# Kernel optimization log

Measured on AMD Instinct MI355X. Metric: run time of the kernel, lower is better.

Reference implementation:

```python
import jax, jax.numpy as jnp
import numpy as np

V, E, H = 32000, 256, 512   # vocab, embed_dim, hidden_dim
B, S, T = 16, 512, 128      # batch, src_len, tgt_len
PAD = 0
H2 = 2 * H                  # decoder hidden size


def setup_inputs() -> dict:
    key = jax.random.key(0)
    ks = jax.random.split(key, 20)
    g = lambda k, shape: jax.random.normal(k, shape, dtype=jnp.float32) * 0.05
    emb = g(ks[0], (V, E)).at[PAD].set(0.0)  # padding_idx row zeroed
    inp = {
        "src": jax.random.randint(ks[18], (B, S), 0, V, dtype=jnp.int32),
        "tgt": jax.random.randint(ks[19], (B, T), 0, V, dtype=jnp.int32),
        "emb": emb,
        # encoder forward direction (torch gate order i,f,g,o)
        "Wih_f": g(ks[1], (4 * H, E)), "Whh_f": g(ks[2], (4 * H, H)),
        "bih_f": g(ks[3], (4 * H,)),   "bhh_f": g(ks[4], (4 * H,)),
        # encoder backward direction
        "Wih_b": g(ks[5], (4 * H, E)), "Whh_b": g(ks[6], (4 * H, H)),
        "bih_b": g(ks[7], (4 * H,)),   "bhh_b": g(ks[8], (4 * H,)),
        # decoder LSTM: input E+2H, hidden 2H
        "Wih_d": g(ks[9], (4 * H2, E + H2)), "Whh_d": g(ks[10], (4 * H2, H2)),
        "bih_d": g(ks[11], (4 * H2,)),       "bhh_d": g(ks[12], (4 * H2,)),
        # attention Linear(4H -> 2H)
        "Wa": g(ks[13], (H2, 2 * H2)), "ba": g(ks[14], (H2,)),
        # output Linear(2H -> V)
        "Wo": g(ks[15], (V, H2)), "bo": g(ks[16], (V,)),
    }
    return inp


def _lstm_cell(x, h, c, Wih, Whh, bih, bhh):
    z = x @ Wih.T + h @ Whh.T + bih + bhh
    i, f, g, o = jnp.split(z, 4, axis=-1)
    c = jax.nn.sigmoid(f) * c + jax.nn.sigmoid(i) * jnp.tanh(g)
    h = jax.nn.sigmoid(o) * jnp.tanh(c)
    return h, c


def _lstm_scan(xs, h0, c0, Wih, Whh, bih, bhh):
    def step(carry, x):
        h, c = _lstm_cell(x, carry[0], carry[1], Wih, Whh, bih, bhh)
        return (h, c), h
    (hT, cT), hs = jax.lax.scan(step, (h0, c0), xs)
    return hs, hT, cT


def reference(src, tgt, emb, Wih_f, Whh_f, bih_f, bhh_f, Wih_b, Whh_b, bih_b, bhh_b,
              Wih_d, Whh_d, bih_d, bhh_d, Wa, ba, Wo, bo):
    z = jnp.zeros((B, H), dtype=emb.dtype)
    xs = emb[src].transpose(1, 0, 2)                       # [S,B,E]
    hs_f, hTf, _ = _lstm_scan(xs,        z, z, Wih_f, Whh_f, bih_f, bhh_f)
    hs_b, hTb, _ = _lstm_scan(xs[::-1],  z, z, Wih_b, Whh_b, bih_b, bhh_b)
    enc_out = jnp.concatenate([hs_f, hs_b[::-1]], -1).transpose(1, 0, 2)  # [B,S,2H]
    h = jnp.concatenate([hTf, hTb], -1)                    # decoder h0 [B,2H]
    c = jnp.zeros_like(h)  # note: original reuses encoder c_n; see combined c0 below
    # original uses c_n (last cells) as decoder c0:
    _, _, cTf = _lstm_scan(xs, z, z, Wih_f, Whh_f, bih_f, bhh_f)[1], None, None
    # recompute cleanly (scan already returned cT above; redo properly):
    hs_f2, hTf2, cTf2 = _lstm_scan(xs,       z, z, Wih_f, Whh_f, bih_f, bhh_f)
    hs_b2, hTb2, cTb2 = _lstm_scan(xs[::-1], z, z, Wih_b, Whh_b, bih_b, bhh_b)
    c = jnp.concatenate([cTf2, cTb2], -1)

    Wa_h, Wa_e = Wa[:, :H2], Wa[:, H2:]
    enc_proj = jnp.einsum('bsd,kd->bsk', enc_out, Wa_e) + ba  # [B,S,2H]

    dec_xs = emb[tgt[:, :T - 1]].transpose(1, 0, 2)        # [T-1,B,E] teacher-forced

    def dec_step(carry, x):
        h, c = carry
        energy = jnp.tanh(enc_proj + (h @ Wa_h.T)[:, None, :])  # [B,S,2H]
        w = jax.nn.softmax(energy.sum(-1), axis=1)              # [B,S]
        ctx = jnp.einsum('bs,bsd->bd', w, enc_out)              # [B,2H]
        xi = jnp.concatenate([x, ctx], -1)                      # [B,E+2H]
        h, c = _lstm_cell(xi, h, c, Wih_d, Whh_d, bih_d, bhh_d)
        pred = h @ Wo.T + bo                                    # [B,V]
        return (h, c), pred

    _, preds = jax.lax.scan(dec_step, (h, c), dec_xs)           # [T-1,B,V]
    outputs = jnp.concatenate(
        [jnp.zeros((B, 1, V), dtype=preds.dtype), preds.transpose(1, 0, 2)], axis=1)
    return outputs
```

## Files before the change

### kernel.cpp

```cpp
#include <hip/hip_runtime.h>

typedef unsigned int uint;
typedef unsigned short ushort;
typedef unsigned long long ull;
typedef __attribute__((ext_vector_type(8))) short bf16x8;
typedef __attribute__((ext_vector_type(4))) float f32x4;

static constexpr int V_ = 32000, E_ = 256, H_ = 512, B_ = 16, S_ = 512, T_ = 128;
static constexpr int H2_ = 1024, G4_ = 2048, D4_ = 4096, KXI_ = 2304;
static constexpr int DSTEPS = T_ - 1;
static constexpr int MD = 2048;
static constexpr int NWG_DEC = 256;
static constexpr float LOG2E = 1.4426950408889634f;
static constexpr int ASTR = 2312;

#define DEVFN __device__ __forceinline__

DEVFN ushort f2bf(float f){ uint u = __builtin_bit_cast(uint, f); u += 0x7fffu + ((u>>16)&1u); return (ushort)(u>>16); }
DEVFN float bf2f(ushort h){ uint u = ((uint)h)<<16; return __builtin_bit_cast(float, u); }
DEVFN float fsig(float x){ float e = __builtin_amdgcn_exp2f(-LOG2E*x); return __builtin_amdgcn_rcpf(1.f+e); }
DEVFN float ftanh(float x){ x = fminf(15.f,fmaxf(-15.f,x)); float e = __builtin_amdgcn_exp2f(2.f*LOG2E*x); return (e-1.f)*__builtin_amdgcn_rcpf(e+1.f); }
DEVFN f32x4 mfma16(bf16x8 a, bf16x8 b, f32x4 c){ return __builtin_amdgcn_mfma_f32_16x16x32_bf16(a,b,c,0,0,0); }

struct ull2v{ ull x, y; };
DEVFN ull ald64(const void* p){ return __hip_atomic_load((const ull*)p, __ATOMIC_RELAXED, __HIP_MEMORY_SCOPE_AGENT); }
DEVFN uint ald32u(const uint* p){ return __hip_atomic_load(p, __ATOMIC_RELAXED, __HIP_MEMORY_SCOPE_AGENT); }
DEVFN float ald_f32(const float* p){ uint v = __hip_atomic_load((const uint*)p, __ATOMIC_RELAXED, __HIP_MEMORY_SCOPE_AGENT); return __builtin_bit_cast(float, v); }
DEVFN bf16x8 ald_bf16x8(const ushort* p){ ull2v v{ald64(p), ald64(p+4)}; return __builtin_bit_cast(bf16x8, v); }
DEVFN void ast32(float* p, float v){ __hip_atomic_store(p, v, __ATOMIC_RELAXED, __HIP_MEMORY_SCOPE_AGENT); }
DEVFN void ast16(ushort* p, ushort v){ __hip_atomic_store(p, v, __ATOMIC_RELAXED, __HIP_MEMORY_SCOPE_AGENT); }
DEVFN void astu(uint* p, uint v){ __hip_atomic_store(p, v, __ATOMIC_RELAXED, __HIP_MEMORY_SCOPE_AGENT); }

DEVFN void gbar(uint* flags, int wgid, int tid, uint& rnd){
  __syncthreads();
  rnd++;
  if (tid==0) astu(flags + wgid, rnd);
  if (tid<256){
    while (ald32u(flags + tid) < rnd) __builtin_amdgcn_s_sleep(1);
  }
  __syncthreads();
}
DEVFN void lbar(uint* lflags, int grp, int mem, int tid, uint& rnd){
  __syncthreads();
  rnd++;
  if (tid==0) astu(lflags + grp*16 + mem, rnd);
  if (tid<16){
    while (ald32u(lflags + grp*16 + tid) < rnd) __builtin_amdgcn_s_sleep(1);
  }
  __syncthreads();
}

__global__ void k_init(uint* __restrict__ flags, ushort* __restrict__ hgf, ushort* __restrict__ hgb){
  int i = blockIdx.x*256 + threadIdx.x;
  if (i < 1024) flags[i] = 0;
  if (i < 2*B_*H_){ hgf[i]=0; hgb[i]=0; }
}

__global__ void k_embed(const int* __restrict__ src, const int* __restrict__ tgt,
                        const float* __restrict__ emb, ushort* __restrict__ Xb, ushort* __restrict__ DXb){
  int r = blockIdx.x, tid = threadIdx.x;
  if (r < S_*B_){
    int s = r>>4, b = r&15;
    int id = src[b*S_+s];
    Xb[(size_t)r*E_+tid] = f2bf(emb[(size_t)id*E_+tid]);
  } else {
    int r2 = r - S_*B_;
    int t = r2>>4, b = r2&15;
    int id = tgt[b*T_+t];
    DXb[(size_t)r2*E_+tid] = f2bf(emb[(size_t)id*E_+tid]);
  }
}

__global__ void k_cvt_encw(const float* __restrict__ src, ushort* __restrict__ dst){
  int d = blockIdx.x;
  int wg = d>>7, r = d&127;
  int w = r>>4, jj=(r>>2)&3, g=r&3;
  int srow = g*H_ + wg*32 + w*4 + jj;
  for (int c = threadIdx.x; c < E_; c += 256)
    dst[(size_t)d*E_ + c] = f2bf(src[(size_t)srow*E_ + c]);
}

__global__ void k_bias_encp(const float* __restrict__ bih, const float* __restrict__ bhh, float* __restrict__ dst){
  int d = blockIdx.x*256 + threadIdx.x;
  int wg = d>>7, r = d&127;
  int w = r>>4, jj=(r>>2)&3, g=r&3;
  int srow = g*H_ + wg*32 + w*4 + jj;
  dst[d] = bih[srow]+bhh[srow];
}

__global__ void k_cvt_decw(const float* __restrict__ Wih_d, const float* __restrict__ Whh_d,
                           ushort* __restrict__ dst){
  int d = blockIdx.x;
  int wg = d>>4, r = d&15, jj = r>>2, g = r&3;
  int srow = g*H2_ + wg*4 + jj;
  for (int c = threadIdx.x; c < KXI_; c += 256){
    float v = (c < E_+H2_) ? Wih_d[(size_t)srow*(E_+H2_) + c] : Whh_d[(size_t)srow*H2_ + (c - (E_+H2_))];
    dst[(size_t)d*KXI_ + c] = f2bf(v);
  }
}

__global__ void k_bias_decp(const float* __restrict__ bih, const float* __restrict__ bhh, float* __restrict__ dst){
  int d = blockIdx.x*256 + threadIdx.x;
  int wg = d>>4, r = d&15, jj = r>>2, g = r&3;
  int srow = g*H2_ + wg*4 + jj;
  dst[d] = bih[srow]+bhh[srow];
}

__global__ void k_cvt_strided(const float* __restrict__ src, ushort* __restrict__ dst,
                              int cols, int sld, int soff, int dld, int doff){
  int r = blockIdx.x;
  for (int c = threadIdx.x; c < cols; c += 256)
    dst[(size_t)r*dld + doff + c] = f2bf(src[(size_t)r*sld + soff + c]);
}

__global__ void k_zero_t0(float* __restrict__ out){
  int i = blockIdx.x*256 + threadIdx.x;
  if (i < B_*V_){ int b = i / V_, v = i - b*V_; out[(size_t)b*T_*V_ + v] = 0.f; }
}

template<int MODE>
__global__ __launch_bounds__(256) void gemm128(const ushort* __restrict__ A, const ushort* __restrict__ Bm,
    const float* __restrict__ bias, void* __restrict__ outp, int M, int N, int K, int Mvalid){
  __shared__ __align__(16) ushort As[128*32];
  __shared__ __align__(16) ushort Bs[128*32];
  int tid = threadIdx.x;
  int wave = tid>>6, lane = tid&63;
  int m0 = blockIdx.y*128, n0 = blockIdx.x*128;
  int wm = wave>>1, wn = wave&1;
  int col = lane&15, rg = lane>>4;
  f32x4 acc[4][4];
  #pragma unroll
  for (int i=0;i<4;i++)
    #pragma unroll
    for (int j=0;j<4;j++) acc[i][j] = {0.f,0.f,0.f,0.f};
  for (int k0=0;k0<K;k0+=32){
    __syncthreads();
    #pragma unroll
    for (int j=0;j<2;j++){
      int li = j*256+tid;
      int row = li>>2, ko = (li&3)*8;
      *(bf16x8*)(As + li*8) = *(const bf16x8*)(A + (size_t)(m0+row)*K + k0 + ko);
      *(bf16x8*)(Bs + li*8) = *(const bf16x8*)(Bm + (size_t)(n0+row)*K + k0 + ko);
    }
    __syncthreads();
    bf16x8 af[4], bfr[4];
    #pragma unroll
    for (int f=0;f<4;f++){
      af[f]  = *(const bf16x8*)(As + (wm*64+f*16+col)*32 + rg*8);
      bfr[f] = *(const bf16x8*)(Bs + (wn*64+f*16+col)*32 + rg*8);
    }
    #pragma unroll
    for (int fm=0;fm<4;fm++)
      #pragma unroll
      for (int fn=0;fn<4;fn++)
        acc[fm][fn] = mfma16(af[fm], bfr[fn], acc[fm][fn]);
  }
  #pragma unroll
  for (int fm=0;fm<4;fm++){
    int mrow = m0 + wm*64 + fm*16 + rg*4;
    #pragma unroll
    for (int fn=0;fn<4;fn++){
      int gcol = n0 + wn*64 + fn*16 + col;
      float bv = bias ? bias[gcol] : 0.f;
      #pragma unroll
      for (int i=0;i<4;i++){
        float v = acc[fm][fn][i] + bv;
        int grow = mrow + i;
        if (MODE==0) ((float*)outp)[(size_t)grow*N + gcol] = v;
        else if (MODE==1) ((ushort*)outp)[(size_t)grow*N + gcol] = f2bf(v);
        else if (MODE==3) ((ushort*)outp)[(size_t)(grow>>4)*(16*2048) + gcol*16 + (grow&15)] = f2bf(v);
        else { if (grow < Mvalid){ int b = grow&15, t = grow>>4;
               ((float*)outp)[(size_t)b*T_*V_ + (size_t)(t+1)*V_ + gcol] = v; } }
      }
    }
  }
}

__global__ __launch_bounds__(512) void k_enc_persist(
    const ushort* __restrict__ Xgf, const ushort* __restrict__ Xgb,
    const float* __restrict__ Whhf, const float* __restrict__ Whhb,
    ushort* __restrict__ enc, ushort* __restrict__ enct,
    ushort* __restrict__ hbuf1, float* __restrict__ cbuf0,
    ushort* __restrict__ hgf, ushort* __restrict__ hgb,
    uint* __restrict__ flags){
  const int dir = blockIdx.x >> 4;
  const int wg  = blockIdx.x & 15;
  const ushort* Xg = dir ? Xgb : Xgf;
  const float* Whh = dir ? Whhb : Whhf;
  ushort* hg = dir ? hgb : hgf;
  uint* ef = flags + 512 + dir*16;
  __shared__ __align__(16) ushort Wlds[128*512];
  __shared__ __align__(16) ushort hls[16*512];
  int tid = threadIdx.x;
  for (int it=0; it<32; ++it){
    int r = it*4 + (tid>>7), ct = tid&127;
    int w_ = r>>4, jj=(r>>2)&3, g=r&3;
    int srow = g*H_ + wg*32 + w_*4 + jj;
    float4 v = *(const float4*)(Whh + (size_t)srow*H_ + ct*4);
    ushort4 o; o.x=f2bf(v.x); o.y=f2bf(v.y); o.z=f2bf(v.z); o.w=f2bf(v.w);
    int byte = (r*1024 + ct*8) ^ ((r&7)<<4);
    *(ushort4*)((char*)Wlds + byte) = o;
  }
  int w = tid>>6, lane = tid&63, colL = lane&15, rg = lane>>4;
  int gg = colL&3;
  uint rnd = 0;
  float cst[4];
  #pragma unroll
  for (int i=0;i<4;i++) cst[i]=0.f;
  __syncthreads();
  for (int t=0;t<S_;++t){
    int pos = dir ? (S_-1-t) : t;
    const ushort* hsrc = hg + (t&1)*B_*H_;
    bf16x8 hv[2];
    #pragma unroll
    for (int k2=0;k2<2;k2++){
      int idx = tid + k2*512;
      hv[k2] = ald_bf16x8(hsrc + (idx>>6)*H_ + (idx&63)*8);
    }
    int colg = wg*128 + w*16 + colL;
    ushort4 xv = *(const ushort4*)(Xg + ((size_t)pos*2048 + colg)*16 + rg*4);
    f32x4 acc;
    acc[0]=bf2f(xv.x); acc[1]=bf2f(xv.y); acc[2]=bf2f(xv.z); acc[3]=bf2f(xv.w);
    #pragma unroll
    for (int k2=0;k2<2;k2++){
      int idx = tid + k2*512;
      int byte = ((idx>>6)*1024 + (idx&63)*16) ^ (((idx>>6)&7)<<4);
      *(bf16x8*)((char*)hls + byte) = hv[k2];
    }
    __syncthreads();
    int rowb = w*16 + colL;
    int base = rowb*1024 + rg*16, xm = (rowb&7)<<4;
    int hbase = colL*1024 + rg*16, hxm = (colL&7)<<4;
    #pragma unroll
    for (int kt=0;kt<16;kt++){
      bf16x8 afv = *(const bf16x8*)((const char*)hls + ((hbase + kt*64) ^ hxm));
      bf16x8 bfv = *(const bf16x8*)((const char*)Wlds + ((base + kt*64) ^ xm));
      acc = mfma16(afv, bfv, acc);
    }
    ushort* hdst = hg + ((t+1)&1)*B_*H_;
    #pragma unroll
    for (int i=0;i<4;i++){
      float v0 = acc[i];
      float v1 = __shfl_xor(v0, 1);
      float v2 = __shfl_xor(v0, 2);
      float v3 = __shfl_xor(v1, 2);
      float zi = gg==0?v0: gg==1?v1: gg==2?v2: v3;
      float zf = (gg^1)==0?v0: (gg^1)==1?v1: (gg^1)==2?v2: v3;
      float zg = (gg^2)==0?v0: (gg^2)==1?v1: (gg^2)==2?v2: v3;
      float zo = (gg^3)==0?v0: (gg^3)==1?v1: (gg^3)==2?v2: v3;
      float cc = fsig(zf)*cst[i] + fsig(zi)*ftanh(zg);
      cst[i] = cc;
      float h = fsig(zo)*ftanh(cc);
      if (gg==0){
        int j = wg*32 + w*4 + (colL>>2);
        int b = rg*4+i;
        ushort hb = f2bf(h);
        enc[((size_t)b*S_ + pos)*H2_ + dir*H_ + j] = hb;
        enct[((size_t)b*H2_ + dir*H_ + j)*S_ + pos] = hb;
        ast16(&hdst[b*H_ + j], hb);
        if (t==S_-1){
          hbuf1[b*H2_ + dir*H_ + j] = hb;
          cbuf0[b*H2_ + dir*H_ + j] = cc;
        }
      }
    }
    if (t != S_-1){
      __syncthreads();
      rnd++;
      if (tid==0) astu(ef + wg, rnd);
      if (tid<16){
        while (ald32u(ef + tid) < rnd) __builtin_amdgcn_s_sleep(1);
      }
      __syncthreads();
    }
  }
}

__global__ __launch_bounds__(512) void k_dec(
    const float* __restrict__ P, const ushort* __restrict__ WaH,
    const ushort* __restrict__ Wd, const float* __restrict__ bsd,
    const ushort* __restrict__ enct, const ushort* __restrict__ DXb,
    const float* __restrict__ cbuf0, ushort* __restrict__ hbuf,
    ushort* __restrict__ ctxbuf, float* __restrict__ qbuf,
    float* __restrict__ scores, ushort* __restrict__ hsd,
    uint* __restrict__ flags){
  __shared__ __align__(16) ushort AB[16*ASTR];
  __shared__ __align__(16) float pr[8*256];
  __shared__ float redz[256];
  __shared__ float qls[1024];
  __shared__ float wls[512];
  __shared__ float part[512];
  __shared__ float red[16];
  __shared__ float cst[64];
  uint* lflags = flags + 256;
  int wgid = blockIdx.x, tid = threadIdx.x;
  int w = tid>>6, lane = tid&63, colL = lane&15, rg = lane>>4;
  uint rnd = 0;
  if (tid < 64){
    int jj = tid>>4, b = tid&15;
    cst[tid] = cbuf0[b*H2_ + wgid*4 + jj];
  }
  for (int st=0; st<DSTEPS; ++st){
    ushort* hprev = hbuf + ((st+1)&1)*B_*H2_;
    if (wgid >= 64 && wgid < 128){
      int n0 = (wgid-64)*16;
      bf16x8 af[4];
      #pragma unroll
      for (int kt=0;kt<4;kt++)
        af[kt] = ald_bf16x8(hprev + colL*H2_ + w*128 + kt*32 + rg*8);
      f32x4 acc = {0.f,0.f,0.f,0.f};
      const ushort* Bp = WaH + (size_t)(n0+colL)*H2_ + w*128 + rg*8;
      #pragma unroll
      for (int kt=0;kt<4;kt++)
        acc = mfma16(af[kt], *(const bf16x8*)(Bp + kt*32), acc);
      *(f32x4*)&pr[w*256 + lane*4] = acc;
      __syncthreads();
      if (tid < 256){
        float s = pr[tid];
        #pragma unroll
        for (int w8=1;w8<8;w8++) s += pr[w8*256 + tid];
        int l = tid>>2, i = tid&3;
        ast32(&qbuf[(size_t)((l>>4)*4 + i)*H2_ + n0 + (l&15)], s);
      }
    }
    gbar(flags, wgid, tid, rnd);
    {
      int b = wgid>>4, wc = wgid&15;
      ull q2 = ald64((const ull*)(qbuf + (size_t)b*H2_) + tid);
      *(ull*)&qls[tid*2] = q2;
      __syncthreads();
      f32x4 qv[4];
      #pragma unroll
      for (int u=0;u<4;u++) qv[u] = *(const f32x4*)&qls[lane*16 + u*4];
      int rbase = b*S_ + wc*32 + w*4;
      #pragma unroll
      for (int rr=0;rr<4;rr++){
        int r = rbase + rr;
        const float4* Pr = (const float4*)(P + (size_t)r*H2_) + lane*4;
        float s = 0.f;
        #pragma unroll
        for (int u=0;u<4;u++){
          float4 pv = Pr[u];
          s += ftanh(pv.x+qv[u][0])+ftanh(pv.y+qv[u][1])+ftanh(pv.z+qv[u][2])+ftanh(pv.w+qv[u][3]);
        }
        #pragma unroll
        for (int o=32;o;o>>=1) s += __shfl_xor(s,o);
        if (lane==0) ast32(&scores[r], s);
      }
    }
    lbar(lflags, wgid>>4, wgid&15, tid, rnd);
    {
      int b = wgid>>4, cc = wgid&15;
      float sc = ald_f32(scores + b*S_ + tid);
      float m = sc;
      #pragma unroll
      for (int o=32;o;o>>=1) m = fmaxf(m, __shfl_xor(m,o));
      if (lane==0) red[w] = m;
      __syncthreads();
      m = red[0];
      #pragma unroll
      for (int k2=1;k2<8;k2++) m = fmaxf(m, red[k2]);
      float e = __builtin_amdgcn_exp2f((sc - m)*LOG2E);
      float ss = e;
      #pragma unroll
      for (int o=32;o;o>>=1) ss += __shfl_xor(ss,o);
      if (lane==0) red[8+w] = ss;
      __syncthreads();
      float tot = red[8];
      #pragma unroll
      for (int k2=9;k2<16;k2++) tot += red[k2];
      wls[tid] = e * __builtin_amdgcn_rcpf(tot);
      __syncthreads();
      int c = cc*64 + (tid&63), sseg = tid>>6;
      const ushort* ep = enct + ((size_t)b*H2_ + c)*S_ + sseg*64;
      float a = 0.f;
      #pragma unroll
      for (int u=0;u<8;u++){
        bf16x8 ev = *(const bf16x8*)(ep + u*8);
        #pragma unroll
        for (int j=0;j<8;j++) a += wls[sseg*64 + u*8 + j] * bf2f((ushort)ev[j]);
      }
      part[tid] = a;
      __syncthreads();
      if (tid < 64){
        float s = part[tid];
        #pragma unroll
        for (int g2=1;g2<8;g2++) s += part[g2*64 + tid];
        ast16(&ctxbuf[b*H2_ + cc*64 + tid], f2bf(s));
      }
    }
    gbar(flags, wgid, tid, rnd);
    {
      { int b3 = tid>>5, seg = tid&31;
        *(bf16x8*)&AB[b3*ASTR + seg*8] = *(const bf16x8*)(DXb + (size_t)(st*16+b3)*E_ + seg*8); }
      bf16x8 rc[4], rh2[4];
      #pragma unroll
      for (int k2=0;k2<4;k2++){
        int idx = tid + k2*512;
        rc[k2]  = ald_bf16x8(ctxbuf + (idx>>7)*H2_ + (idx&127)*8);
        rh2[k2] = ald_bf16x8(hprev  + (idx>>7)*H2_ + (idx&127)*8);
      }
      #pragma unroll
      for (int k2=0;k2<4;k2++){
        int idx = tid + k2*512;
        int row = idx>>7, seg = idx&127;
        *(bf16x8*)&AB[row*ASTR + 256 + seg*8]  = rc[k2];
        *(bf16x8*)&AB[row*ASTR + 1280 + seg*8] = rh2[k2];
      }
      __syncthreads();
      int row0 = wgid*16;
      f32x4 acc = {0.f,0.f,0.f,0.f};
      const ushort* Bp = Wd + (size_t)(row0+colL)*KXI_ + w*288 + rg*8;
      const ushort* Apb = &AB[colL*ASTR + w*288 + rg*8];
      #pragma unroll
      for (int kt=0;kt<9;kt++)
        acc = mfma16(*(const bf16x8*)(Apb + kt*32), *(const bf16x8*)(Bp + kt*32), acc);
      *(f32x4*)&pr[w*256 + lane*4] = acc;
      __syncthreads();
      if (tid < 256){
        float s = bsd[row0 + ((tid>>2)&15)];
        #pragma unroll
        for (int w8=0;w8<8;w8++) s += pr[w8*256 + tid];
        redz[tid] = s;
      }
      __syncthreads();
      if (tid < 64){
        int jj = tid>>4, b4 = tid&15, rgc = b4>>2, ic = b4&3;
        float zi = redz[((jj*4+0) + 16*rgc)*4 + ic];
        float zf = redz[((jj*4+1) + 16*rgc)*4 + ic];
        float zg = redz[((jj*4+2) + 16*rgc)*4 + ic];
        float zo = redz[((jj*4+3) + 16*rgc)*4 + ic];
        float cc2 = fsig(zf)*cst[tid] + fsig(zi)*ftanh(zg);
        cst[tid] = cc2;
        float h = fsig(zo)*ftanh(cc2);
        ushort hb = f2bf(h);
        int j = wgid*4 + jj;
        ast16(&(hbuf + (st&1)*B_*H2_)[b4*H2_ + j], hb);
        hsd[((size_t)st*B_ + b4)*H2_ + j] = hb;
      }
      __syncthreads();
    }
    if (st != DSTEPS-1) gbar(flags, wgid, tid, rnd);
  }
}

extern "C" void kernel_launch(void* const* d_in, const int* in_sizes, int n_in,
                              void* d_out, int out_size, void* d_ws, size_t ws_size,
                              hipStream_t stream) {
  const int* src   = (const int*)d_in[0];
  const int* tgt   = (const int*)d_in[1];
  const float* emb   = (const float*)d_in[2];
  const float* Wih_f = (const float*)d_in[3];
  const float* Whh_f = (const float*)d_in[4];
  const float* bih_f = (const float*)d_in[5];
  const float* bhh_f = (const float*)d_in[6];
  const float* Wih_b = (const float*)d_in[7];
  const float* Whh_b = (const float*)d_in[8];
  const float* bih_b = (const float*)d_in[9];
  const float* bhh_b = (const float*)d_in[10];
  const float* Wih_d = (const float*)d_in[11];
  const float* Whh_d = (const float*)d_in[12];
  const float* bih_d = (const float*)d_in[13];
  const float* bhh_d = (const float*)d_in[14];
  const float* Wa    = (const float*)d_in[15];
  const float* ba    = (const float*)d_in[16];
  const float* Wo    = (const float*)d_in[17];
  const float* bo    = (const float*)d_in[18];
  float* out = (float*)d_out;
  (void)in_sizes; (void)n_in; (void)out_size; (void)ws_size;

  char* ws = (char*)d_ws;
  size_t off = 0;
  auto alloc = [&](size_t bytes)->char*{ char* p = ws + off; off += (bytes + 255) & ~(size_t)255; return p; };
  ushort* Xb     = (ushort*)alloc((size_t)S_*B_*E_*2);
  ushort* DXb    = (ushort*)alloc((size_t)DSTEPS*B_*E_*2);
  ushort* Wihf_p = (ushort*)alloc((size_t)G4_*E_*2);
  ushort* Wihb_p = (ushort*)alloc((size_t)G4_*E_*2);
  float*  bsf    = (float*)alloc(G4_*4);
  float*  bsb    = (float*)alloc(G4_*4);
  ushort* ENC    = (ushort*)alloc((size_t)B_*S_*H2_*2);
  ushort* ENCT   = (ushort*)alloc((size_t)B_*S_*H2_*2);
  ushort* WaH    = (ushort*)alloc((size_t)H2_*H2_*2);
  ushort* WaE    = (ushort*)alloc((size_t)H2_*H2_*2);
  ushort* Wd     = (ushort*)alloc((size_t)D4_*KXI_*2);
  float*  bsd    = (float*)alloc(D4_*4);
  ushort* WoB    = (ushort*)alloc((size_t)V_*H2_*2);
  float*  cbuf0  = (float*)alloc(B_*H2_*4);
  ushort* hbuf   = (ushort*)alloc((size_t)2*B_*H2_*2);
  ushort* ctxbuf = (ushort*)alloc((size_t)B_*H2_*2);
  float*  qbuf   = (float*)alloc(B_*H2_*4);
  float*  scores = (float*)alloc(B_*S_*4);
  ushort* hsd    = (ushort*)alloc((size_t)MD*H2_*2);
  ushort* hgf    = (ushort*)alloc((size_t)2*B_*H_*2);
  ushort* hgb    = (ushort*)alloc((size_t)2*B_*H_*2);
  uint*   flags  = (uint*)alloc(4096);
  char*   big    = alloc((size_t)2*S_*B_*G4_*2);
  ushort* Xgf = (ushort*)big;
  ushort* Xgb = (ushort*)(big + (size_t)S_*B_*G4_*2);
  float*  P   = (float*)big;

  k_init<<<dim3(64), dim3(256), 0, stream>>>(flags, hgf, hgb);
  k_embed<<<dim3(S_*B_ + DSTEPS*B_), dim3(E_), 0, stream>>>(src, tgt, emb, Xb, DXb);
  k_cvt_encw<<<dim3(G4_), dim3(256), 0, stream>>>(Wih_f, Wihf_p);
  k_cvt_encw<<<dim3(G4_), dim3(256), 0, stream>>>(Wih_b, Wihb_p);
  k_bias_encp<<<dim3(8), dim3(256), 0, stream>>>(bih_f, bhh_f, bsf);
  k_bias_encp<<<dim3(8), dim3(256), 0, stream>>>(bih_b, bhh_b, bsb);
  k_cvt_strided<<<dim3(H2_), dim3(256), 0, stream>>>(Wa, WaH, H2_, 2*H2_, 0,   H2_, 0);
  k_cvt_strided<<<dim3(H2_), dim3(256), 0, stream>>>(Wa, WaE, H2_, 2*H2_, H2_, H2_, 0);
  k_cvt_decw<<<dim3(D4_), dim3(256), 0, stream>>>(Wih_d, Whh_d, Wd);
  k_bias_decp<<<dim3(16), dim3(256), 0, stream>>>(bih_d, bhh_d, bsd);
  k_cvt_strided<<<dim3(V_),  dim3(256), 0, stream>>>(Wo, WoB, H2_, H2_, 0, H2_, 0);

  gemm128<3><<<dim3(G4_/128, (S_*B_)/128), dim3(256), 0, stream>>>(Xb, Wihf_p, bsf, Xgf, S_*B_, G4_, E_, 0);
  gemm128<3><<<dim3(G4_/128, (S_*B_)/128), dim3(256), 0, stream>>>(Xb, Wihb_p, bsb, Xgb, S_*B_, G4_, E_, 0);

  k_enc_persist<<<dim3(32), dim3(512), 0, stream>>>(Xgf, Xgb, Whh_f, Whh_b, ENC, ENCT,
                                                    hbuf + B_*H2_, cbuf0, hgf, hgb, flags);

  gemm128<0><<<dim3(H2_/128, (B_*S_)/128), dim3(256), 0, stream>>>(ENC, WaE, ba, P, B_*S_, H2_, H2_, 0);
  k_zero_t0<<<dim3((B_*V_+255)/256), dim3(256), 0, stream>>>(out);

  k_dec<<<dim3(NWG_DEC), dim3(512), 0, stream>>>(P, WaH, Wd, bsd, ENCT, DXb, cbuf0, hbuf,
                                                 ctxbuf, qbuf, scores, hsd, flags);

  gemm128<2><<<dim3(V_/128, MD/128), dim3(256), 0, stream>>>(hsd, WoB, bo, out, MD, V_, H2_, DSTEPS*B_);
}
```

Measured before the change: 6.252 ms.

## Redistribute attention query projection and split barriers to prefetch across grid syncs

The Wa_h·h query projection, previously done by 64 workgroups followed by a grid-wide barrier, is now computed redundantly per batch group so that only a local 16-workgroup barrier is needed. That removes one global barrier per decoder step. Barriers are split into arrive and wait phases so that loads of P rows, encoder values and decoder weight fragments are issued between them, hiding memory latency behind the synchronisation wait. This costs more register pressure (large prefetch arrays) and redundant scalar dot-product work on the query projection.

```diff
diff --git a/kernel.cpp b/kernel.cpp
--- a/kernel.cpp
+++ b/kernel.cpp
@@ -30,25 +30,6 @@
 DEVFN void ast32(float* p, float v){ __hip_atomic_store(p, v, __ATOMIC_RELAXED, __HIP_MEMORY_SCOPE_AGENT); }
 DEVFN void ast16(ushort* p, ushort v){ __hip_atomic_store(p, v, __ATOMIC_RELAXED, __HIP_MEMORY_SCOPE_AGENT); }
 DEVFN void astu(uint* p, uint v){ __hip_atomic_store(p, v, __ATOMIC_RELAXED, __HIP_MEMORY_SCOPE_AGENT); }
-
-DEVFN void gbar(uint* flags, int wgid, int tid, uint& rnd){
-  __syncthreads();
-  rnd++;
-  if (tid==0) astu(flags + wgid, rnd);
-  if (tid<256){
-    while (ald32u(flags + tid) < rnd) __builtin_amdgcn_s_sleep(1);
-  }
-  __syncthreads();
-}
-DEVFN void lbar(uint* lflags, int grp, int mem, int tid, uint& rnd){
-  __syncthreads();
-  rnd++;
-  if (tid==0) astu(lflags + grp*16 + mem, rnd);
-  if (tid<16){
-    while (ald32u(lflags + grp*16 + tid) < rnd) __builtin_amdgcn_s_sleep(1);
-  }
-  __syncthreads();
-}
 
 __global__ void k_init(uint* __restrict__ flags, ushort* __restrict__ hgf, ushort* __restrict__ hgb){
   int i = blockIdx.x*256 + threadIdx.x;
@@ -295,37 +276,68 @@
   uint* lflags = flags + 256;
   int wgid = blockIdx.x, tid = threadIdx.x;
   int w = tid>>6, lane = tid&63, colL = lane&15, rg = lane>>4;
+  int b = wgid>>4, wc = wgid&15;
   uint rnd = 0;
   if (tid < 64){
-    int jj = tid>>4, b = tid&15;
-    cst[tid] = cbuf0[b*H2_ + wgid*4 + jj];
+    int jj = tid>>4, b4 = tid&15;
+    cst[tid] = cbuf0[b4*H2_ + wgid*4 + jj];
   }
   for (int st=0; st<DSTEPS; ++st){
     ushort* hprev = hbuf + ((st+1)&1)*B_*H2_;
-    if (wgid >= 64 && wgid < 128){
-      int n0 = (wgid-64)*16;
-      bf16x8 af[4];
-      #pragma unroll
-      for (int kt=0;kt<4;kt++)
-        af[kt] = ald_bf16x8(hprev + colL*H2_ + w*128 + kt*32 + rg*8);
-      f32x4 acc = {0.f,0.f,0.f,0.f};
-      const ushort* Bp = WaH + (size_t)(n0+colL)*H2_ + w*128 + rg*8;
-      #pragma unroll
-      for (int kt=0;kt<4;kt++)
-        acc = mfma16(af[kt], *(const bf16x8*)(Bp + kt*32), acc);
-      *(f32x4*)&pr[w*256 + lane*4] = acc;
-      __syncthreads();
-      if (tid < 256){
-        float s = pr[tid];
-        #pragma unroll
-        for (int w8=1;w8<8;w8++) s += pr[w8*256 + tid];
-        int l = tid>>2, i = tid&3;
-        ast32(&qbuf[(size_t)((l>>4)*4 + i)*H2_ + n0 + (l&15)], s);
-      }
-    }
-    gbar(flags, wgid, tid, rnd);
-    {
-      int b = wgid>>4, wc = wgid&15;
+    { int b3 = tid>>5, seg = tid&31;
+      *(bf16x8*)&AB[b3*ASTR + seg*8] = *(const bf16x8*)(DXb + (size_t)(st*16+b3)*E_ + seg*8); }
+    {
+      bf16x8 rh2[4];
+      #pragma unroll
+      for (int k2=0;k2<4;k2++){
+        int idx = tid + k2*512;
+        rh2[k2] = ald_bf16x8(hprev + (idx>>7)*H2_ + (idx&127)*8);
+      }
+      #pragma unroll
+      for (int k2=0;k2<4;k2++){
+        int idx = tid + k2*512;
+        *(bf16x8*)&AB[(idx>>7)*ASTR + 1280 + (idx&127)*8] = rh2[k2];
+      }
+    }
+    __syncthreads();
+    {
+      int nl = tid&63, kc = tid>>6;
+      int n = wc*64 + nl;
+      const ushort* wp = WaH + (size_t)n*H2_ + kc*128;
+      const ushort* hp = &AB[b*ASTR + 1280 + kc*128];
+      float s = 0.f;
+      #pragma unroll
+      for (int u=0;u<16;u++){
+        bf16x8 wv = *(const bf16x8*)(wp + u*8);
+        bf16x8 hv = *(const bf16x8*)(hp + u*8);
+        #pragma unroll
+        for (int j=0;j<8;j++) s += bf2f((ushort)wv[j]) * bf2f((ushort)hv[j]);
+      }
+      part[kc*64 + nl] = s;
+      __syncthreads();
+      if (tid < 64){
+        float q = 0.f;
+        #pragma unroll
+        for (int c2=0;c2<8;c2++) q += part[c2*64 + tid];
+        ast32(&qbuf[(size_t)b*H2_ + wc*64 + tid], q);
+      }
+    }
+    __syncthreads();
+    rnd++;
+    if (tid==0) astu(lflags + b*16 + wc, rnd);
+    f32x4 pv[16];
+    {
+      int rbase = b*S_ + wc*32 + w*4;
+      #pragma unroll
+      for (int rr=0;rr<4;rr++){
+        const f32x4* Pr = (const f32x4*)(P + (size_t)(rbase+rr)*H2_) + lane*4;
+        #pragma unroll
+        for (int u=0;u<4;u++) pv[rr*4+u] = Pr[u];
+      }
+    }
+    if (tid<16){ while (ald32u(lflags + b*16 + tid) < rnd) __builtin_amdgcn_s_sleep(1); }
+    __syncthreads();
+    {
       ull q2 = ald64((const ull*)(qbuf + (size_t)b*H2_) + tid);
       *(ull*)&qls[tid*2] = q2;
       __syncthreads();
@@ -335,22 +347,30 @@
       int rbase = b*S_ + wc*32 + w*4;
       #pragma unroll
       for (int rr=0;rr<4;rr++){
-        int r = rbase + rr;
-        const float4* Pr = (const float4*)(P + (size_t)r*H2_) + lane*4;
         float s = 0.f;
         #pragma unroll
         for (int u=0;u<4;u++){
-          float4 pv = Pr[u];
-          s += ftanh(pv.x+qv[u][0])+ftanh(pv.y+qv[u][1])+ftanh(pv.z+qv[u][2])+ftanh(pv.w+qv[u][3]);
+          f32x4 p4 = pv[rr*4+u];
+          s += ftanh(p4[0]+qv[u][0])+ftanh(p4[1]+qv[u][1])+ftanh(p4[2]+qv[u][2])+ftanh(p4[3]+qv[u][3]);
         }
         #pragma unroll
         for (int o=32;o;o>>=1) s += __shfl_xor(s,o);
-        if (lane==0) ast32(&scores[r], s);
-      }
-    }
-    lbar(lflags, wgid>>4, wgid&15, tid, rnd);
-    {
-      int b = wgid>>4, cc = wgid&15;
+        if (lane==0) ast32(&scores[rbase+rr], s);
+      }
+    }
+    __syncthreads();
+    rnd++;
+    if (tid==0) astu(lflags + b*16 + wc, rnd);
+    bf16x8 ev[8];
+    {
+      int c = wc*64 + (tid&63), sseg = tid>>6;
+      const ushort* ep = enct + ((size_t)b*H2_ + c)*S_ + sseg*64;
+      #pragma unroll
+      for (int u=0;u<8;u++) ev[u] = *(const bf16x8*)(ep + u*8);
+    }
+    if (tid<16){ while (ald32u(lflags + b*16 + tid) < rnd) __builtin_amdgcn_s_sleep(1); }
+    __syncthreads();
+    {
       float sc = ald_f32(scores + b*S_ + tid);
       float m = sc;
       #pragma unroll
@@ -371,14 +391,12 @@
       for (int k2=9;k2<16;k2++) tot += red[k2];
       wls[tid] = e * __builtin_amdgcn_rcpf(tot);
       __syncthreads();
-      int c = cc*64 + (tid&63), sseg = tid>>6;
-      const ushort* ep = enct + ((size_t)b*H2_ + c)*S_ + sseg*64;
+      int sseg = tid>>6;
       float a = 0.f;
       #pragma unroll
       for (int u=0;u<8;u++){
-        bf16x8 ev = *(const bf16x8*)(ep + u*8);
-        #pragma unroll
-        for (int j=0;j<8;j++) a += wls[sseg*64 + u*8 + j] * bf2f((ushort)ev[j]);
+        #pragma unroll
+        for (int j=0;j<8;j++) a += wls[sseg*64 + u*8 + j] * bf2f((ushort)ev[u][j]);
       }
       part[tid] = a;
       __syncthreads();
@@ -386,35 +404,40 @@
         float s = part[tid];
         #pragma unroll
         for (int g2=1;g2<8;g2++) s += part[g2*64 + tid];
-        ast16(&ctxbuf[b*H2_ + cc*64 + tid], f2bf(s));
-      }
-    }
-    gbar(flags, wgid, tid, rnd);
-    {
-      { int b3 = tid>>5, seg = tid&31;
-        *(bf16x8*)&AB[b3*ASTR + seg*8] = *(const bf16x8*)(DXb + (size_t)(st*16+b3)*E_ + seg*8); }
-      bf16x8 rc[4], rh2[4];
+        ast16(&ctxbuf[b*H2_ + wc*64 + tid], f2bf(s));
+      }
+    }
+    __syncthreads();
+    rnd++;
+    if (tid==0) astu(flags + wgid, rnd);
+    bf16x8 bw[9];
+    {
+      int row0 = wgid*16;
+      const ushort* Bp = Wd + (size_t)(row0+colL)*KXI_ + w*288 + rg*8;
+      #pragma unroll
+      for (int kt=0;kt<9;kt++) bw[kt] = *(const bf16x8*)(Bp + kt*32);
+    }
+    if (tid<256){ while (ald32u(flags + tid) < rnd) __builtin_amdgcn_s_sleep(1); }
+    __syncthreads();
+    {
+      bf16x8 rc[4];
       #pragma unroll
       for (int k2=0;k2<4;k2++){
         int idx = tid + k2*512;
-        rc[k2]  = ald_bf16x8(ctxbuf + (idx>>7)*H2_ + (idx&127)*8);
-        rh2[k2] = ald_bf16x8(hprev  + (idx>>7)*H2_ + (idx&127)*8);
+        rc[k2] = ald_bf16x8(ctxbuf + (idx>>7)*H2_ + (idx&127)*8);
       }
       #pragma unroll
       for (int k2=0;k2<4;k2++){
         int idx = tid + k2*512;
-        int row = idx>>7, seg = idx&127;
-        *(bf16x8*)&AB[row*ASTR + 256 + seg*8]  = rc[k2];
-        *(bf16x8*)&AB[row*ASTR + 1280 + seg*8] = rh2[k2];
+        *(bf16x8*)&AB[(idx>>7)*ASTR + 256 + (idx&127)*8] = rc[k2];
       }
       __syncthreads();
       int row0 = wgid*16;
       f32x4 acc = {0.f,0.f,0.f,0.f};
-      const ushort* Bp = Wd + (size_t)(row0+colL)*KXI_ + w*288 + rg*8;
       const ushort* Apb = &AB[colL*ASTR + w*288 + rg*8];
       #pragma unroll
       for (int kt=0;kt<9;kt++)
-        acc = mfma16(*(const bf16x8*)(Apb + kt*32), *(const bf16x8*)(Bp + kt*32), acc);
+        acc = mfma16(*(const bf16x8*)(Apb + kt*32), bw[kt], acc);
       *(f32x4*)&pr[w*256 + lane*4] = acc;
       __syncthreads();
       if (tid < 256){
@@ -438,9 +461,14 @@
         ast16(&(hbuf + (st&1)*B_*H2_)[b4*H2_ + j], hb);
         hsd[((size_t)st*B_ + b4)*H2_ + j] = hb;
       }
-      __syncthreads();
-    }
-    if (st != DSTEPS-1) gbar(flags, wgid, tid, rnd);
+    }
+    if (st != DSTEPS-1){
+      __syncthreads();
+      rnd++;
+      if (tid==0) astu(flags + wgid, rnd);
+      if (tid<256){ while (ald32u(flags + tid) < rnd) __builtin_amdgcn_s_sleep(1); }
+      __syncthreads();
+    }
   }
 }
 
```

Result: slower. 8.431 ms (+34.9%).

## Fuse attention scores with partial context via split-softmax, drop transposed encoder copy

Applied to the files above, without the earlier changes.

Each decoder workgroup now computes its 32 attention scores, a local max, local exp-sum and an unnormalized partial context over those rows straight from the row-major encoder output. The partial results and statistics go to global memory. After the local barrier the partials are merged with flash-style rescaling to form the normalized context. This removes the global scores round trip and the serialized softmax phase. It also removes the transposed encoder copy, which the encoder kernel wrote with strided stores. In exchange it adds more LDS (a 32KB partial buffer) and a 16-way merge of partial contexts read from global memory each step.

```diff
diff --git a/kernel.cpp b/kernel.cpp
--- a/kernel.cpp
+++ b/kernel.cpp
@@ -179,7 +179,7 @@
 __global__ __launch_bounds__(512) void k_enc_persist(
     const ushort* __restrict__ Xgf, const ushort* __restrict__ Xgb,
     const float* __restrict__ Whhf, const float* __restrict__ Whhb,
-    ushort* __restrict__ enc, ushort* __restrict__ enct,
+    ushort* __restrict__ enc,
     ushort* __restrict__ hbuf1, float* __restrict__ cbuf0,
     ushort* __restrict__ hgf, ushort* __restrict__ hgb,
     uint* __restrict__ flags){
@@ -256,7 +256,6 @@
         int b = rg*4+i;
         ushort hb = f2bf(h);
         enc[((size_t)b*S_ + pos)*H2_ + dir*H_ + j] = hb;
-        enct[((size_t)b*H2_ + dir*H_ + j)*S_ + pos] = hb;
         ast16(&hdst[b*H_ + j], hb);
         if (t==S_-1){
           hbuf1[b*H2_ + dir*H_ + j] = hb;
@@ -279,26 +278,29 @@
 __global__ __launch_bounds__(512) void k_dec(
     const float* __restrict__ P, const ushort* __restrict__ WaH,
     const ushort* __restrict__ Wd, const float* __restrict__ bsd,
-    const ushort* __restrict__ enct, const ushort* __restrict__ DXb,
+    const ushort* __restrict__ enc, const ushort* __restrict__ DXb,
     const float* __restrict__ cbuf0, ushort* __restrict__ hbuf,
     ushort* __restrict__ ctxbuf, float* __restrict__ qbuf,
-    float* __restrict__ scores, ushort* __restrict__ hsd,
-    uint* __restrict__ flags){
+    float* __restrict__ ctxp, float* __restrict__ statml, float* __restrict__ statse,
+    ushort* __restrict__ hsd, uint* __restrict__ flags){
   __shared__ __align__(16) ushort AB[16*ASTR];
   __shared__ __align__(16) float pr[8*256];
+  __shared__ __align__(16) float pp[8*1024];
   __shared__ float redz[256];
   __shared__ float qls[1024];
-  __shared__ float wls[512];
-  __shared__ float part[512];
-  __shared__ float red[16];
+  __shared__ float sls[32];
+  __shared__ float red2[8];
+  __shared__ float mls[16];
+  __shared__ float ses[16];
   __shared__ float cst[64];
   uint* lflags = flags + 256;
   int wgid = blockIdx.x, tid = threadIdx.x;
   int w = tid>>6, lane = tid&63, colL = lane&15, rg = lane>>4;
+  int b = wgid>>4, wc = wgid&15;
   uint rnd = 0;
   if (tid < 64){
-    int jj = tid>>4, b = tid&15;
-    cst[tid] = cbuf0[b*H2_ + wgid*4 + jj];
+    int jj = tid>>4, b4 = tid&15;
+    cst[tid] = cbuf0[b4*H2_ + wgid*4 + jj];
   }
   for (int st=0; st<DSTEPS; ++st){
     ushort* hprev = hbuf + ((st+1)&1)*B_*H2_;
@@ -325,18 +327,16 @@
     }
     gbar(flags, wgid, tid, rnd);
     {
-      int b = wgid>>4, wc = wgid&15;
       ull q2 = ald64((const ull*)(qbuf + (size_t)b*H2_) + tid);
       *(ull*)&qls[tid*2] = q2;
       __syncthreads();
       f32x4 qv[4];
       #pragma unroll
       for (int u=0;u<4;u++) qv[u] = *(const f32x4*)&qls[lane*16 + u*4];
-      int rbase = b*S_ + wc*32 + w*4;
+      int sbase = wc*32 + w*4;
       #pragma unroll
       for (int rr=0;rr<4;rr++){
-        int r = rbase + rr;
-        const float4* Pr = (const float4*)(P + (size_t)r*H2_) + lane*4;
+        const float4* Pr = (const float4*)(P + (size_t)(b*S_ + sbase+rr)*H2_) + lane*4;
         float s = 0.f;
         #pragma unroll
         for (int u=0;u<4;u++){
@@ -345,48 +345,66 @@
         }
         #pragma unroll
         for (int o=32;o;o>>=1) s += __shfl_xor(s,o);
-        if (lane==0) ast32(&scores[r], s);
-      }
-    }
-    lbar(lflags, wgid>>4, wgid&15, tid, rnd);
+        if (lane==0) sls[w*4+rr] = s;
+      }
+      __syncthreads();
+      float ml = sls[0];
+      #pragma unroll
+      for (int i2=1;i2<32;i2++) ml = fmaxf(ml, sls[i2]);
+      float a[16];
+      #pragma unroll
+      for (int j=0;j<16;j++) a[j] = 0.f;
+      float se = 0.f;
+      #pragma unroll
+      for (int rr=0;rr<4;rr++){
+        float wgt = __builtin_amdgcn_exp2f((sls[w*4+rr]-ml)*LOG2E);
+        se += wgt;
+        const ushort* er = enc + ((size_t)(b*S_ + sbase+rr))*H2_ + lane*16;
+        bf16x8 e0 = *(const bf16x8*)er;
+        bf16x8 e1 = *(const bf16x8*)(er+8);
+        #pragma unroll
+        for (int j=0;j<8;j++){
+          a[j]   += wgt*bf2f((ushort)e0[j]);
+          a[8+j] += wgt*bf2f((ushort)e1[j]);
+        }
+      }
+      #pragma unroll
+      for (int u=0;u<4;u++)
+        *(f32x4*)&pp[w*1024 + lane*16 + u*4] = *(f32x4*)&a[u*4];
+      if (lane==0) red2[w] = se;
+      __syncthreads();
+      { int c2 = tid*2;
+        float c0=0.f, c1=0.f;
+        #pragma unroll
+        for (int w8=0;w8<8;w8++){ c0 += pp[w8*1024 + c2]; c1 += pp[w8*1024 + c2+1]; }
+        ast32(&ctxp[((size_t)b*16 + wc)*H2_ + c2], c0);
+        ast32(&ctxp[((size_t)b*16 + wc)*H2_ + c2+1], c1);
+      }
+      if (tid==0){
+        float t2 = 0.f;
+        #pragma unroll
+        for (int w8=0;w8<8;w8++) t2 += red2[w8];
+        ast32(&statml[b*16+wc], ml);
+        ast32(&statse[b*16+wc], t2);
+      }
+    }
+    lbar(lflags, b, wc, tid, rnd);
     {
-      int b = wgid>>4, cc = wgid&15;
-      float sc = ald_f32(scores + b*S_ + tid);
-      float m = sc;
-      #pragma unroll
-      for (int o=32;o;o>>=1) m = fmaxf(m, __shfl_xor(m,o));
-      if (lane==0) red[w] = m;
-      __syncthreads();
-      m = red[0];
-      #pragma unroll
-      for (int k2=1;k2<8;k2++) m = fmaxf(m, red[k2]);
-      float e = __builtin_amdgcn_exp2f((sc - m)*LOG2E);
-      float ss = e;
-      #pragma unroll
-      for (int o=32;o;o>>=1) ss += __shfl_xor(ss,o);
-      if (lane==0) red[8+w] = ss;
-      __syncthreads();
-      float tot = red[8];
-      #pragma unroll
-      for (int k2=9;k2<16;k2++) tot += red[k2];
-      wls[tid] = e * __builtin_amdgcn_rcpf(tot);
-      __syncthreads();
-      int c = cc*64 + (tid&63), sseg = tid>>6;
-      const ushort* ep = enct + ((size_t)b*H2_ + c)*S_ + sseg*64;
-      float a = 0.f;
-      #pragma unroll
-      for (int u=0;u<8;u++){
-        bf16x8 ev = *(const bf16x8*)(ep + u*8);
-        #pragma unroll
-        for (int j=0;j<8;j++) a += wls[sseg*64 + u*8 + j] * bf2f((ushort)ev[j]);
-      }
-      part[tid] = a;
+      if (tid<16){ mls[tid] = ald_f32(&statml[b*16+tid]); ses[tid] = ald_f32(&statse[b*16+tid]); }
       __syncthreads();
       if (tid < 64){
-        float s = part[tid];
-        #pragma unroll
-        for (int g2=1;g2<8;g2++) s += part[g2*64 + tid];
-        ast16(&ctxbuf[b*H2_ + cc*64 + tid], f2bf(s));
+        float M = mls[0];
+        #pragma unroll
+        for (int g=1;g<16;g++) M = fmaxf(M, mls[g]);
+        float fg[16]; float tot = 0.f;
+        #pragma unroll
+        for (int g=0;g<16;g++){ fg[g] = __builtin_amdgcn_exp2f((mls[g]-M)*LOG2E); tot += ses[g]*fg[g]; }
+        float rinv = __builtin_amdgcn_rcpf(tot);
+        int c = wc*64 + tid;
+        float s = 0.f;
+        #pragma unroll
+        for (int g=0;g<16;g++) s += ald_f32(&ctxp[((size_t)b*16+g)*H2_ + c]) * fg[g];
+        ast16(&ctxbuf[b*H2_ + c], f2bf(s*rinv));
       }
     }
     gbar(flags, wgid, tid, rnd);
@@ -479,7 +497,6 @@
   float*  bsf    = (float*)alloc(G4_*4);
   float*  bsb    = (float*)alloc(G4_*4);
   ushort* ENC    = (ushort*)alloc((size_t)B_*S_*H2_*2);
-  ushort* ENCT   = (ushort*)alloc((size_t)B_*S_*H2_*2);
   ushort* WaH    = (ushort*)alloc((size_t)H2_*H2_*2);
   ushort* WaE    = (ushort*)alloc((size_t)H2_*H2_*2);
   ushort* Wd     = (ushort*)alloc((size_t)D4_*KXI_*2);
@@ -489,7 +506,9 @@
   ushort* hbuf   = (ushort*)alloc((size_t)2*B_*H2_*2);
   ushort* ctxbuf = (ushort*)alloc((size_t)B_*H2_*2);
   float*  qbuf   = (float*)alloc(B_*H2_*4);
-  float*  scores = (float*)alloc(B_*S_*4);
+  float*  ctxp   = (float*)alloc((size_t)B_*16*H2_*4);
+  float*  statml = (float*)alloc(256*4);
+  float*  statse = (float*)alloc(256*4);
   ushort* hsd    = (ushort*)alloc((size_t)MD*H2_*2);
   ushort* hgf    = (ushort*)alloc((size_t)2*B_*H_*2);
   ushort* hgb    = (ushort*)alloc((size_t)2*B_*H_*2);
@@ -514,14 +533,14 @@
   gemm128<3><<<dim3(G4_/128, (S_*B_)/128), dim3(256), 0, stream>>>(Xb, Wihf_p, bsf, Xgf, S_*B_, G4_, E_, 0);
   gemm128<3><<<dim3(G4_/128, (S_*B_)/128), dim3(256), 0, stream>>>(Xb, Wihb_p, bsb, Xgb, S_*B_, G4_, E_, 0);
 
-  k_enc_persist<<<dim3(32), dim3(512), 0, stream>>>(Xgf, Xgb, Whh_f, Whh_b, ENC, ENCT,
+  k_enc_persist<<<dim3(32), dim3(512), 0, stream>>>(Xgf, Xgb, Whh_f, Whh_b, ENC,
                                                     hbuf + B_*H2_, cbuf0, hgf, hgb, flags);
 
   gemm128<0><<<dim3(H2_/128, (B_*S_)/128), dim3(256), 0, stream>>>(ENC, WaE, ba, P, B_*S_, H2_, H2_, 0);
   k_zero_t0<<<dim3((B_*V_+255)/256), dim3(256), 0, stream>>>(out);
 
-  k_dec<<<dim3(NWG_DEC), dim3(512), 0, stream>>>(P, WaH, Wd, bsd, ENCT, DXb, cbuf0, hbuf,
-                                                 ctxbuf, qbuf, scores, hsd, flags);
+  k_dec<<<dim3(NWG_DEC), dim3(512), 0, stream>>>(P, WaH, Wd, bsd, ENC, DXb, cbuf0, hbuf,
+                                                 ctxbuf, qbuf, ctxp, statml, statse, hsd, flags);
 
   gemm128<2><<<dim3(V_/128, MD/128), dim3(256), 0, stream>>>(hsd, WoB, bo, out, MD, V_, H2_, DSTEPS*B_);
 }
```

New measurement: 6.823 ms. +9.1%, slower.

## Replace decoder grid barriers with step-tagged data flags on h and ctx

Applied to the files above, without the earlier changes.

Two of the three grid-wide barriers per decoder step are removed. Each bf16 value of the hidden state and context is now stored in a 32-bit word whose high half holds the step index, and consumers spin on those tags until every element they need carries the expected step. The q buffer is double-buffered so it does not race across steps. This cuts the barrier latency on the serial decoder recurrence, at the cost of twice the memory traffic for h and ctx plus repeated polling reads.

```diff
diff --git a/kernel.cpp b/kernel.cpp
--- a/kernel.cpp
+++ b/kernel.cpp
@@ -50,10 +50,12 @@
   __syncthreads();
 }
 
-__global__ void k_init(uint* __restrict__ flags, ushort* __restrict__ hgf, ushort* __restrict__ hgb){
+__global__ void k_init(uint* __restrict__ flags, ushort* __restrict__ hgf, ushort* __restrict__ hgb,
+                       uint* __restrict__ hU, uint* __restrict__ ctxU){
   int i = blockIdx.x*256 + threadIdx.x;
   if (i < 1024) flags[i] = 0;
   if (i < 2*B_*H_){ hgf[i]=0; hgb[i]=0; }
+  if (i < B_*H2_){ hU[i] = 0u; ctxU[i] = 0u; }
 }
 
 __global__ void k_embed(const int* __restrict__ src, const int* __restrict__ tgt,
@@ -180,7 +182,7 @@
     const ushort* __restrict__ Xgf, const ushort* __restrict__ Xgb,
     const float* __restrict__ Whhf, const float* __restrict__ Whhb,
     ushort* __restrict__ enc, ushort* __restrict__ enct,
-    ushort* __restrict__ hbuf1, float* __restrict__ cbuf0,
+    uint* __restrict__ hbuf1, float* __restrict__ cbuf0,
     ushort* __restrict__ hgf, ushort* __restrict__ hgb,
     uint* __restrict__ flags){
   const int dir = blockIdx.x >> 4;
@@ -259,7 +261,7 @@
         enct[((size_t)b*H2_ + dir*H_ + j)*S_ + pos] = hb;
         ast16(&hdst[b*H_ + j], hb);
         if (t==S_-1){
-          hbuf1[b*H2_ + dir*H_ + j] = hb;
+          hbuf1[b*H2_ + dir*H_ + j] = (uint)hb;
           cbuf0[b*H2_ + dir*H_ + j] = cc;
         }
       }
@@ -280,8 +282,8 @@
     const float* __restrict__ P, const ushort* __restrict__ WaH,
     const ushort* __restrict__ Wd, const float* __restrict__ bsd,
     const ushort* __restrict__ enct, const ushort* __restrict__ DXb,
-    const float* __restrict__ cbuf0, ushort* __restrict__ hbuf,
-    ushort* __restrict__ ctxbuf, float* __restrict__ qbuf,
+    const float* __restrict__ cbuf0, uint* __restrict__ hU,
+    uint* __restrict__ ctxU, float* __restrict__ qbuf,
     float* __restrict__ scores, ushort* __restrict__ hsd,
     uint* __restrict__ flags){
   __shared__ __align__(16) ushort AB[16*ASTR];
@@ -295,24 +297,44 @@
   uint* lflags = flags + 256;
   int wgid = blockIdx.x, tid = threadIdx.x;
   int w = tid>>6, lane = tid&63, colL = lane&15, rg = lane>>4;
+  int b = wgid>>4, wc = wgid&15;
   uint rnd = 0;
   if (tid < 64){
-    int jj = tid>>4, b = tid&15;
-    cst[tid] = cbuf0[b*H2_ + wgid*4 + jj];
+    int jj = tid>>4, b4 = tid&15;
+    cst[tid] = cbuf0[b4*H2_ + wgid*4 + jj];
   }
   for (int st=0; st<DSTEPS; ++st){
-    ushort* hprev = hbuf + ((st+1)&1)*B_*H2_;
+    const uint* hprevU = hU + ((st+1)&1)*B_*H2_;
+    const uint wantH = (uint)st;
+    const uint wantC = (uint)(st+1);
+    float* qslot = qbuf + (st&1)*B_*H2_;
     if (wgid >= 64 && wgid < 128){
       int n0 = (wgid-64)*16;
-      bf16x8 af[4];
-      #pragma unroll
-      for (int kt=0;kt<4;kt++)
-        af[kt] = ald_bf16x8(hprev + colL*H2_ + w*128 + kt*32 + rg*8);
+      const uint* hp = hprevU + colL*H2_ + w*128 + rg*8;
+      uint uu[32];
+      for(;;){
+        #pragma unroll
+        for (int kt=0;kt<4;kt++)
+          #pragma unroll
+          for (int j=0;j<4;j++){
+            ull v = ald64(hp + kt*32 + j*2);
+            uu[kt*8+j*2] = (uint)v; uu[kt*8+j*2+1] = (uint)(v>>32);
+          }
+        bool ok = true;
+        #pragma unroll
+        for (int i2=0;i2<32;i2++) ok &= ((uu[i2]>>16) == wantH);
+        if (ok) break;
+        __builtin_amdgcn_s_sleep(1);
+      }
       f32x4 acc = {0.f,0.f,0.f,0.f};
       const ushort* Bp = WaH + (size_t)(n0+colL)*H2_ + w*128 + rg*8;
       #pragma unroll
-      for (int kt=0;kt<4;kt++)
-        acc = mfma16(af[kt], *(const bf16x8*)(Bp + kt*32), acc);
+      for (int kt=0;kt<4;kt++){
+        ushort tmp[8];
+        #pragma unroll
+        for (int j=0;j<8;j++) tmp[j] = (ushort)uu[kt*8+j];
+        acc = mfma16(*(bf16x8*)tmp, *(const bf16x8*)(Bp + kt*32), acc);
+      }
       *(f32x4*)&pr[w*256 + lane*4] = acc;
       __syncthreads();
       if (tid < 256){
@@ -320,13 +342,12 @@
         #pragma unroll
         for (int w8=1;w8<8;w8++) s += pr[w8*256 + tid];
         int l = tid>>2, i = tid&3;
-        ast32(&qbuf[(size_t)((l>>4)*4 + i)*H2_ + n0 + (l&15)], s);
+        ast32(&qslot[(size_t)((l>>4)*4 + i)*H2_ + n0 + (l&15)], s);
       }
     }
     gbar(flags, wgid, tid, rnd);
     {
-      int b = wgid>>4, wc = wgid&15;
-      ull q2 = ald64((const ull*)(qbuf + (size_t)b*H2_) + tid);
+      ull q2 = ald64((const ull*)(qslot + (size_t)b*H2_) + tid);
       *(ull*)&qls[tid*2] = q2;
       __syncthreads();
       f32x4 qv[4];
@@ -348,9 +369,8 @@
         if (lane==0) ast32(&scores[r], s);
       }
     }
-    lbar(lflags, wgid>>4, wgid&15, tid, rnd);
+    lbar(lflags, b, wc, tid, rnd);
     {
-      int b = wgid>>4, cc = wgid&15;
       float sc = ald_f32(scores + b*S_ + tid);
       float m = sc;
       #pragma unroll
@@ -371,7 +391,7 @@
       for (int k2=9;k2<16;k2++) tot += red[k2];
       wls[tid] = e * __builtin_amdgcn_rcpf(tot);
       __syncthreads();
-      int c = cc*64 + (tid&63), sseg = tid>>6;
+      int c = wc*64 + (tid&63), sseg = tid>>6;
       const ushort* ep = enct + ((size_t)b*H2_ + c)*S_ + sseg*64;
       float a = 0.f;
       #pragma unroll
@@ -386,26 +406,67 @@
         float s = part[tid];
         #pragma unroll
         for (int g2=1;g2<8;g2++) s += part[g2*64 + tid];
-        ast16(&ctxbuf[b*H2_ + cc*64 + tid], f2bf(s));
-      }
-    }
-    gbar(flags, wgid, tid, rnd);
+        astu(&ctxU[b*H2_ + wc*64 + tid], (uint)f2bf(s) | (wantC<<16));
+      }
+    }
     {
       { int b3 = tid>>5, seg = tid&31;
         *(bf16x8*)&AB[b3*ASTR + seg*8] = *(const bf16x8*)(DXb + (size_t)(st*16+b3)*E_ + seg*8); }
-      bf16x8 rc[4], rh2[4];
-      #pragma unroll
-      for (int k2=0;k2<4;k2++){
-        int idx = tid + k2*512;
-        rc[k2]  = ald_bf16x8(ctxbuf + (idx>>7)*H2_ + (idx&127)*8);
-        rh2[k2] = ald_bf16x8(hprev  + (idx>>7)*H2_ + (idx&127)*8);
-      }
-      #pragma unroll
-      for (int k2=0;k2<4;k2++){
-        int idx = tid + k2*512;
-        int row = idx>>7, seg = idx&127;
-        *(bf16x8*)&AB[row*ASTR + 256 + seg*8]  = rc[k2];
-        *(bf16x8*)&AB[row*ASTR + 1280 + seg*8] = rh2[k2];
+      {
+        uint uu[32];
+        for(;;){
+          #pragma unroll
+          for (int k2=0;k2<4;k2++){
+            int idx = tid + k2*512;
+            const uint* p = ctxU + (idx>>7)*H2_ + (idx&127)*8;
+            #pragma unroll
+            for (int j=0;j<4;j++){
+              ull v = ald64(p + j*2);
+              uu[k2*8+j*2] = (uint)v; uu[k2*8+j*2+1] = (uint)(v>>32);
+            }
+          }
+          bool ok = true;
+          #pragma unroll
+          for (int i2=0;i2<32;i2++) ok &= ((uu[i2]>>16) == wantC);
+          if (ok) break;
+          __builtin_amdgcn_s_sleep(1);
+        }
+        #pragma unroll
+        for (int k2=0;k2<4;k2++){
+          int idx = tid + k2*512;
+          ushort tmp[8];
+          #pragma unroll
+          for (int j=0;j<8;j++) tmp[j] = (ushort)uu[k2*8+j];
+          *(bf16x8*)&AB[(idx>>7)*ASTR + 256 + (idx&127)*8] = *(bf16x8*)tmp;
+        }
+      }
+      {
+        uint uu[32];
+        for(;;){
+          #pragma unroll
+          for (int k2=0;k2<4;k2++){
+            int idx = tid + k2*512;
+            const uint* p = hprevU + (idx>>7)*H2_ + (idx&127)*8;
+            #pragma unroll
+            for (int j=0;j<4;j++){
+              ull v = ald64(p + j*2);
+              uu[k2*8+j*2] = (uint)v; uu[k2*8+j*2+1] = (uint)(v>>32);
+            }
+          }
+          bool ok = true;
+          #pragma unroll
+          for (int i2=0;i2<32;i2++) ok &= ((uu[i2]>>16) == wantH);
+          if (ok) break;
+          __builtin_amdgcn_s_sleep(1);
+        }
+        #pragma unroll
+        for (int k2=0;k2<4;k2++){
+          int idx = tid + k2*512;
+          ushort tmp[8];
+          #pragma unroll
+          for (int j=0;j<8;j++) tmp[j] = (ushort)uu[k2*8+j];
+          *(bf16x8*)&AB[(idx>>7)*ASTR + 1280 + (idx&127)*8] = *(bf16x8*)tmp;
+        }
       }
       __syncthreads();
       int row0 = wgid*16;
@@ -435,12 +496,11 @@
         float h = fsig(zo)*ftanh(cc2);
         ushort hb = f2bf(h);
         int j = wgid*4 + jj;
-        ast16(&(hbuf + (st&1)*B_*H2_)[b4*H2_ + j], hb);
+        astu(&hU[(st&1)*B_*H2_ + b4*H2_ + j], (uint)hb | ((uint)(st+1)<<16));
         hsd[((size_t)st*B_ + b4)*H2_ + j] = hb;
       }
       __syncthreads();
     }
-    if (st != DSTEPS-1) gbar(flags, wgid, tid, rnd);
   }
 }
 
@@ -486,9 +546,9 @@
   float*  bsd    = (float*)alloc(D4_*4);
   ushort* WoB    = (ushort*)alloc((size_t)V_*H2_*2);
   float*  cbuf0  = (float*)alloc(B_*H2_*4);
-  ushort* hbuf   = (ushort*)alloc((size_t)2*B_*H2_*2);
-  ushort* ctxbuf = (ushort*)alloc((size_t)B_*H2_*2);
-  float*  qbuf   = (float*)alloc(B_*H2_*4);
+  uint*   hU     = (uint*)alloc((size_t)2*B_*H2_*4);
+  uint*   ctxU   = (uint*)alloc((size_t)B_*H2_*4);
+  float*  qbuf   = (float*)alloc((size_t)2*B_*H2_*4);
   float*  scores = (float*)alloc(B_*S_*4);
   ushort* hsd    = (ushort*)alloc((size_t)MD*H2_*2);
   ushort* hgf    = (ushort*)alloc((size_t)2*B_*H_*2);
@@ -499,7 +559,7 @@
   ushort* Xgb = (ushort*)(big + (size_t)S_*B_*G4_*2);
   float*  P   = (float*)big;
 
-  k_init<<<dim3(64), dim3(256), 0, stream>>>(flags, hgf, hgb);
+  k_init<<<dim3(64), dim3(256), 0, stream>>>(flags, hgf, hgb, hU, ctxU);
   k_embed<<<dim3(S_*B_ + DSTEPS*B_), dim3(E_), 0, stream>>>(src, tgt, emb, Xb, DXb);
   k_cvt_encw<<<dim3(G4_), dim3(256), 0, stream>>>(Wih_f, Wihf_p);
   k_cvt_encw<<<dim3(G4_), dim3(256), 0, stream>>>(Wih_b, Wihb_p);
@@ -515,13 +575,13 @@
   gemm128<3><<<dim3(G4_/128, (S_*B_)/128), dim3(256), 0, stream>>>(Xb, Wihb_p, bsb, Xgb, S_*B_, G4_, E_, 0);
 
   k_enc_persist<<<dim3(32), dim3(512), 0, stream>>>(Xgf, Xgb, Whh_f, Whh_b, ENC, ENCT,
-                                                    hbuf + B_*H2_, cbuf0, hgf, hgb, flags);
+                                                    hU + B_*H2_, cbuf0, hgf, hgb, flags);
 
   gemm128<0><<<dim3(H2_/128, (B_*S_)/128), dim3(256), 0, stream>>>(ENC, WaE, ba, P, B_*S_, H2_, H2_, 0);
   k_zero_t0<<<dim3((B_*V_+255)/256), dim3(256), 0, stream>>>(out);
 
-  k_dec<<<dim3(NWG_DEC), dim3(512), 0, stream>>>(P, WaH, Wd, bsd, ENCT, DXb, cbuf0, hbuf,
-                                                 ctxbuf, qbuf, scores, hsd, flags);
+  k_dec<<<dim3(NWG_DEC), dim3(512), 0, stream>>>(P, WaH, Wd, bsd, ENCT, DXb, cbuf0, hU,
+                                                 ctxU, qbuf, scores, hsd, flags);
 
   gemm128<2><<<dim3(V_/128, MD/128), dim3(256), 0, stream>>>(hsd, WoB, bo, out, MD, V_, H2_, DSTEPS*B_);
 }
```

Result: faster. 6.039 ms (-3.4%).
